# Performance work log

Hardware: AMD Instinct MI355X
Metric: run time of the kernel (lower is better)

The kernel has to match this reference:

```python
import jax, jax.numpy as jnp
import numpy as np

B, S, D = 4, 1024, 1024      # batch, seq_len, hidden_size
I = 4096                     # intermediate_size
E = 8                        # num_experts
K = 2                        # top-k


def setup_inputs() -> dict:
    key = jax.random.key(0)
    ks = jax.random.split(key, 8)
    x = jax.random.normal(ks[0], (B, S, D), dtype=jnp.float32)
    gate_w = jax.random.normal(ks[1], (E, D), dtype=jnp.float32) * 0.02
    gate_b = jnp.zeros((E,), dtype=jnp.float32)
    w1 = jax.random.normal(ks[2], (E, I, D), dtype=jnp.float32) * 0.02
    b1 = jnp.zeros((E, I), dtype=jnp.float32)
    w2 = jax.random.normal(ks[3], (E, D, I), dtype=jnp.float32) * 0.02
    b2 = jnp.zeros((E, D), dtype=jnp.float32)
    return {"x": x, "gate_w": gate_w, "gate_b": gate_b,
            "w1": w1, "b1": b1, "w2": w2, "b2": b2}


def reference(x, gate_w, gate_b, w1, b1, w2, b2):
    b, s, d = x.shape
    xf = x.reshape(-1, d)                                  # [N, D]
    logits = xf @ gate_w.T + gate_b                        # [N, E]
    top_vals, top_idx = jax.lax.top_k(logits, K)           # [N, K]
    top_w = jax.nn.softmax(top_vals, axis=-1)              # softmax over the k selected logits

    # combine[n, e] = routing weight of token n for expert e (0 if not selected)
    n_tok = xf.shape[0]
    combine = jnp.zeros((n_tok, w1.shape[0]), dtype=x.dtype)
    combine = combine.at[jnp.arange(n_tok)[:, None], top_idx].add(top_w)

    out = jnp.zeros_like(xf)
    for e in range(w1.shape[0]):                           # small fixed loop over experts
        h = jax.nn.gelu(xf @ w1[e].T + b1[e], approximate=False)  # exact GELU (torch default)
        out = out + combine[:, e:e + 1] * (h @ w2[e].T + b2[e])
    return out.reshape(b, s, d)
```

## Files before the change

### kernel.cpp

```cpp
#include <hip/hip_runtime.h>
#include <math.h>

#define NTOK 4096
#define DDIM 1024
#define IDIM 4096
#define NEXP 8
#define MAXPAD 9216

typedef _Float16 f16x8 __attribute__((ext_vector_type(8)));
typedef _Float16 f16x4 __attribute__((ext_vector_type(4)));
typedef float    f32x4 __attribute__((ext_vector_type(4)));

__device__ __forceinline__ void glds16(const _Float16* g, _Float16* l) {
    __builtin_amdgcn_global_load_lds(
        (const __attribute__((address_space(1))) _Float16*)g,
        (__attribute__((address_space(3))) _Float16*)l, 16, 0, 0);
}

__device__ __forceinline__ float fast_gelu(float v) {
    float u = v * (0.7978845608f + 0.0356774081f * v * v);
    float ex = __builtin_amdgcn_exp2f(u * 2.8853900817779268f);
    float th = 1.0f - 2.0f * __builtin_amdgcn_rcpf(ex + 1.0f);
    return 0.5f * v * (1.0f + th);
}

__global__ void cvt_kernel(const float* __restrict__ src, _Float16* __restrict__ dst, int n4) {
    int i = blockIdx.x * blockDim.x + threadIdx.x;
    if (i >= n4) return;
    float4 v = ((const float4*)src)[i];
    f16x4 o = { (_Float16)v.x, (_Float16)v.y, (_Float16)v.z, (_Float16)v.w };
    ((f16x4*)dst)[i] = o;
}

__global__ void gate_kernel(const float* __restrict__ x, const float* __restrict__ gw,
                            const float* __restrict__ gb,
                            int* __restrict__ cnt, int* __restrict__ tok,
                            float* __restrict__ wgt) {
    int wave = threadIdx.x >> 6;
    int lane = threadIdx.x & 63;
    int token = blockIdx.x * 4 + wave;
    const float* xr = x + (size_t)token * DDIM;
    float xv[16];
#pragma unroll
    for (int j = 0; j < 16; ++j) xv[j] = xr[lane + 64 * j];
    float lg[NEXP];
#pragma unroll
    for (int e = 0; e < NEXP; ++e) {
        const float* g = gw + e * DDIM;
        float s = 0.f;
#pragma unroll
        for (int j = 0; j < 16; ++j) s += xv[j] * g[lane + 64 * j];
#pragma unroll
        for (int o = 32; o > 0; o >>= 1) s += __shfl_xor(s, o, 64);
        lg[e] = s + gb[e];
    }
    if (lane == 0) {
        int i0 = 0; float v0 = lg[0];
        for (int e = 1; e < NEXP; ++e) if (lg[e] > v0) { v0 = lg[e]; i0 = e; }
        int i1 = -1; float v1 = -3.0e38f;
        for (int e = 0; e < NEXP; ++e) { if (e == i0) continue; if (lg[e] > v1) { v1 = lg[e]; i1 = e; } }
        float e1 = expf(v1 - v0);
        float den = 1.f + e1;
        float w0 = 1.f / den;
        float w1 = e1 / den;
        int p0 = atomicAdd(&cnt[i0], 1);
        tok[i0 * NTOK + p0] = token; wgt[i0 * NTOK + p0] = w0;
        int p1 = atomicAdd(&cnt[i1], 1);
        tok[i1 * NTOK + p1] = token; wgt[i1 * NTOK + p1] = w1;
    }
}

__global__ void scan_kernel(const int* __restrict__ cnt, int* __restrict__ off,
                            int* __restrict__ q1, int* __restrict__ q2) {
    if (threadIdx.x == 0) {
        int acc = 0;
        for (int e = 0; e < NEXP; ++e) { off[e] = acc; acc += ((cnt[e] + 127) >> 7) << 7; }
        off[NEXP] = acc;
        int n1 = 0, n2 = 0;
        for (int e = 0; e < NEXP; ++e) {
            int mtiles = (cnt[e] + 255) >> 8;
            for (int mt = 0; mt < mtiles; ++mt) {
                for (int nt = 0; nt < IDIM / 256; ++nt)
                    q1[n1++] = e | (mt << 4) | (nt << 12);
                for (int kc = 0; kc < 4; ++kc)
                    for (int nt = 0; nt < DDIM / 256; ++nt)
                        q2[n2++] = e | (mt << 4) | (nt << 12) | (kc << 20);
            }
        }
        off[10] = n1; off[11] = n2;
    }
}

__global__ void gather_kernel(const float* __restrict__ x, const int* __restrict__ cnt,
                              const int* __restrict__ off, const int* __restrict__ tok,
                              _Float16* __restrict__ xg) {
    int row = blockIdx.x;
    if (row >= off[NEXP]) return;
    int e = 0;
    while (e < NEXP - 1 && row >= off[e + 1]) ++e;
    int r = row - off[e];
    int t = threadIdx.x;
    _Float16* dst = xg + (size_t)row * DDIM;
    if (r < cnt[e]) {
        int token = tok[e * NTOK + r];
        float4 v = ((const float4*)(x + (size_t)token * DDIM))[t];
        f16x4 o = { (_Float16)v.x, (_Float16)v.y, (_Float16)v.z, (_Float16)v.w };
        ((f16x4*)dst)[t] = o;
    } else {
        f16x4 z = {};
        ((f16x4*)dst)[t] = z;
    }
}

#define SBAR() do { __builtin_amdgcn_s_barrier(); asm volatile("" ::: "memory"); } while (0)
#define STA(b, s, ko) glds16(ap[s] + (ko), &As[b][((s) * 64 + wv * 8) * 64])
#define STB(b, s, ko) glds16(bp[s] + (ko), &Bs[b][((s) * 64 + wv * 8) * 64])
#define ARD(buf, row, kb) (*(const f16x8*)&As[buf][(row) * 64 + ((((kb) + fq) ^ ((row) & 7)) << 3)])
#define BRD(buf, row, kb) (*(const f16x8*)&Bs[buf][(row) * 64 + ((((kb) + fq) ^ ((row) & 7)) << 3)])

template <int KDIM, int NDIM, int EPI, int SPLIT>
__global__ __launch_bounds__(512, 2) void gemm256_kernel(
    const _Float16* __restrict__ A,
    const _Float16* __restrict__ Bw,
    const float* __restrict__ bias,
    const int* __restrict__ cnt, const int* __restrict__ off,
    const int* __restrict__ tok, const float* __restrict__ wgt,
    _Float16* __restrict__ Hout, float* __restrict__ Out,
    const int* __restrict__ qarr, const int* __restrict__ qn) {
    constexpr int KB = KDIM / SPLIT;
    constexpr int NK = KB / 64;

    __shared__ __align__(16) _Float16 As[2][256 * 64];
    __shared__ __align__(16) _Float16 Bs[2][256 * 64];

    const int tid = threadIdx.x;
    const int wv = tid >> 6, lane = tid & 63;
    const int wm = (wv >> 2) * 128;
    const int wn = (wv & 3) * 64;
    const int fr = lane & 15, fq = lane >> 4;
    const int srow = lane >> 3;
    const int scol = ((lane & 7) ^ srow) << 3;
    const int nwork = *qn;

    for (int wi = blockIdx.x; wi < nwork; wi += gridDim.x) {
        __syncthreads();
        const int w = qarr[wi];
        const int e  = w & 15;
        const int mt = (w >> 4) & 63;
        const int nt = (w >> 12) & 63;
        const int kc = (w >> 20) & 7;
        const int ce = cnt[e];
        const int rowbase = off[e] + mt * 256;
        const int colbase = nt * 256;

        const _Float16* ap[4];
        const _Float16* bp[4];
#pragma unroll
        for (int s = 0; s < 4; ++s) {
            int ra = rowbase + s * 64 + wv * 8 + srow;
            if (ra > MAXPAD - 1) ra = MAXPAD - 1;
            ap[s] = A + (size_t)ra * KDIM + kc * KB + scol;
            bp[s] = Bw + ((size_t)e * NDIM + colbase + s * 64 + wv * 8 + srow) * KDIM + kc * KB + scol;
        }

        f32x4 acc[8][4] = {};

        STA(0, 0, 0); STA(0, 1, 0); STA(0, 2, 0); STA(0, 3, 0);
        STB(0, 0, 0); STB(0, 1, 0); STB(0, 2, 0); STB(0, 3, 0);

        for (int kt = 0; kt < NK; ++kt) {
            const int cur = kt & 1, nxt = cur ^ 1;
            const int ko = (kt + 1) * 64;
            f16x8 a[4], b[4];
            if (kt + 1 < NK) {
                STA(nxt, 0, ko); STA(nxt, 1, ko); STA(nxt, 2, ko); STA(nxt, 3, ko);
                STB(nxt, 0, ko); STB(nxt, 1, ko); STB(nxt, 2, ko); STB(nxt, 3, ko);
                asm volatile("s_waitcnt vmcnt(8)" ::: "memory");
            } else {
                asm volatile("s_waitcnt vmcnt(0)" ::: "memory");
            }
            SBAR();
#pragma unroll
            for (int i = 0; i < 4; ++i) a[i] = ARD(cur, wm + i * 16 + fr, 0);
#pragma unroll
            for (int j = 0; j < 4; ++j) b[j] = BRD(cur, wn + j * 16 + fr, 0);
            __builtin_amdgcn_s_setprio(1);
#pragma unroll
            for (int i = 0; i < 4; ++i)
#pragma unroll
                for (int j = 0; j < 4; ++j)
                    acc[i][j] = __builtin_amdgcn_mfma_f32_16x16x32_f16(a[i], b[j], acc[i][j], 0, 0, 0);
            __builtin_amdgcn_s_setprio(0);
#pragma unroll
            for (int i = 0; i < 4; ++i) a[i] = ARD(cur, wm + 64 + i * 16 + fr, 0);
            __builtin_amdgcn_s_setprio(1);
#pragma unroll
            for (int i = 0; i < 4; ++i)
#pragma unroll
                for (int j = 0; j < 4; ++j)
                    acc[i + 4][j] = __builtin_amdgcn_mfma_f32_16x16x32_f16(a[i], b[j], acc[i + 4][j], 0, 0, 0);
            __builtin_amdgcn_s_setprio(0);
#pragma unroll
            for (int i = 0; i < 4; ++i) a[i] = ARD(cur, wm + 64 + i * 16 + fr, 4);
#pragma unroll
            for (int j = 0; j < 4; ++j) b[j] = BRD(cur, wn + j * 16 + fr, 4);
            __builtin_amdgcn_s_setprio(1);
#pragma unroll
            for (int i = 0; i < 4; ++i)
#pragma unroll
                for (int j = 0; j < 4; ++j)
                    acc[i + 4][j] = __builtin_amdgcn_mfma_f32_16x16x32_f16(a[i], b[j], acc[i + 4][j], 0, 0, 0);
            __builtin_amdgcn_s_setprio(0);
#pragma unroll
            for (int i = 0; i < 4; ++i) a[i] = ARD(cur, wm + i * 16 + fr, 4);
            __builtin_amdgcn_s_setprio(1);
#pragma unroll
            for (int i = 0; i < 4; ++i)
#pragma unroll
                for (int j = 0; j < 4; ++j)
                    acc[i][j] = __builtin_amdgcn_mfma_f32_16x16x32_f16(a[i], b[j], acc[i][j], 0, 0, 0);
            __builtin_amdgcn_s_setprio(0);
            asm volatile("s_waitcnt lgkmcnt(0)" ::: "memory");
            SBAR();
        }

        const int rq = fq << 2;
        if constexpr (EPI == 1) {
            const int elim = off[e + 1];
#pragma unroll
            for (int q = 0; q < 8; ++q) {
                const int rbase = wm + ((q >> 2) * 64) + ((q & 3) * 16) + rq;
#pragma unroll
                for (int r = 0; r < 4; ++r) {
                    const int grow = rowbase + rbase + r;
                    if (grow < elim) {
#pragma unroll
                        for (int j = 0; j < 4; ++j) {
                            const int col = colbase + wn + j * 16 + fr;
                            float v = fast_gelu(acc[q][j][r] + bias[e * NDIM + col]);
                            Hout[(size_t)grow * NDIM + col] = (_Float16)v;
                        }
                    }
                }
            }
        } else {
#pragma unroll
            for (int q = 0; q < 8; ++q) {
                const int rbase = wm + ((q >> 2) * 64) + ((q & 3) * 16) + rq;
#pragma unroll
                for (int r = 0; r < 4; ++r) {
                    const int slot = mt * 256 + rbase + r;
                    if (slot < ce) {
                        const int token = tok[e * NTOK + slot];
                        const float ww = wgt[e * NTOK + slot];
#pragma unroll
                        for (int j = 0; j < 4; ++j) {
                            const int col = colbase + wn + j * 16 + fr;
                            float v = acc[q][j][r];
                            if (kc == 0) v += bias[e * NDIM + col];
                            unsafeAtomicAdd(&Out[(size_t)token * NDIM + col], ww * v);
                        }
                    }
                }
            }
        }
    }
}

extern "C" void kernel_launch(void* const* d_in, const int* in_sizes, int n_in,
                              void* d_out, int out_size, void* d_ws, size_t ws_size,
                              hipStream_t stream) {
    const float* x      = (const float*)d_in[0];
    const float* gate_w = (const float*)d_in[1];
    const float* gate_b = (const float*)d_in[2];
    const float* w1     = (const float*)d_in[3];
    const float* b1     = (const float*)d_in[4];
    const float* w2     = (const float*)d_in[5];
    const float* b2     = (const float*)d_in[6];
    float* out = (float*)d_out;

    char* p = (char*)d_ws;
    _Float16* w1h  = (_Float16*)p; p += (size_t)NEXP * IDIM * DDIM * 2;
    _Float16* w2h  = (_Float16*)p; p += (size_t)NEXP * DDIM * IDIM * 2;
    _Float16* xg   = (_Float16*)p; p += (size_t)MAXPAD * DDIM * 2;
    _Float16* hbuf = (_Float16*)p; p += (size_t)MAXPAD * IDIM * 2;
    int*      tok  = (int*)p;      p += (size_t)NEXP * NTOK * 4;
    float*    wgt  = (float*)p;    p += (size_t)NEXP * NTOK * 4;
    int*      cnt  = (int*)p;      p += 128;
    int*      off  = (int*)p;      p += 128;
    int*      q1   = (int*)p;      p += 4096;
    int*      q2   = (int*)p;      p += 4096;

    hipMemsetAsync(cnt, 0, 128, stream);
    hipMemsetAsync(out, 0, (size_t)NTOK * DDIM * 4, stream);

    cvt_kernel<<<32768, 256, 0, stream>>>(w1, w1h, NEXP * IDIM * DDIM / 4);
    cvt_kernel<<<32768, 256, 0, stream>>>(w2, w2h, NEXP * DDIM * IDIM / 4);
    gate_kernel<<<NTOK / 4, 256, 0, stream>>>(x, gate_w, gate_b, cnt, tok, wgt);
    scan_kernel<<<1, 64, 0, stream>>>(cnt, off, q1, q2);
    gather_kernel<<<MAXPAD, 256, 0, stream>>>(x, cnt, off, tok, xg);

    gemm256_kernel<DDIM, IDIM, 1, 1><<<dim3(256), 512, 0, stream>>>(
        xg, w1h, b1, cnt, off, tok, wgt, hbuf, (float*)nullptr, q1, off + 10);
    gemm256_kernel<IDIM, DDIM, 2, 4><<<dim3(256), 512, 0, stream>>>(
        hbuf, w2h, b2, cnt, off, tok, wgt, (_Float16*)nullptr, out, q2, off + 11);
}
```

Measured before the change: 842.2 us.

## Use 16-wave blocks with 4-stage K=32 LDS pipeline in expert GEMMs

Restructures the grouped GEMM to launch 1024 threads (16 waves), each owning a 64x64 sub-tile of the 256x256 block instead of 128x64. It also halves the K slice to 32, with a 4-deep ring of LDS buffers and three stages prefetched, using an adjusted XOR swizzle. The aim is to hide global-load latency with deeper prefetch and to cut per-wave accumulator registers for more latency tolerance. In exchange each wave does less MFMA work per barrier, so barriers per unit of work roughly double. The fixed-count vmcnt waits also depend on each wave issuing exactly two loads per stage.

```diff
diff --git a/kernel.cpp b/kernel.cpp
--- a/kernel.cpp
+++ b/kernel.cpp
@@ -113,13 +113,15 @@
 }
 
 #define SBAR() do { __builtin_amdgcn_s_barrier(); asm volatile("" ::: "memory"); } while (0)
-#define STA(b, s, ko) glds16(ap[s] + (ko), &As[b][((s) * 64 + wv * 8) * 64])
-#define STB(b, s, ko) glds16(bp[s] + (ko), &Bs[b][((s) * 64 + wv * 8) * 64])
-#define ARD(buf, row, kb) (*(const f16x8*)&As[buf][(row) * 64 + ((((kb) + fq) ^ ((row) & 7)) << 3)])
-#define BRD(buf, row, kb) (*(const f16x8*)&Bs[buf][(row) * 64 + ((((kb) + fq) ^ ((row) & 7)) << 3)])
+#define STAGE(b, ko) do { \
+    glds16(ap + (ko), &As[b][wv * 512]); \
+    glds16(bp + (ko), &Bs[b][wv * 512]); \
+} while (0)
+#define ARD(buf, r) (*(const f16x8*)&As[buf][(r) * 32 + ((fq ^ (((r) >> 1) & 3)) << 3)])
+#define BRD(buf, r) (*(const f16x8*)&Bs[buf][(r) * 32 + ((fq ^ (((r) >> 1) & 3)) << 3)])
 
 template <int KDIM, int NDIM, int EPI, int SPLIT>
-__global__ __launch_bounds__(512, 2) void gemm256_kernel(
+__global__ __launch_bounds__(1024, 4) void gemm256_kernel(
     const _Float16* __restrict__ A,
     const _Float16* __restrict__ Bw,
     const float* __restrict__ bias,
@@ -128,91 +130,54 @@
     _Float16* __restrict__ Hout, float* __restrict__ Out,
     const int* __restrict__ qarr, const int* __restrict__ qn) {
     constexpr int KB = KDIM / SPLIT;
-    constexpr int NK = KB / 64;
-
-    __shared__ __align__(16) _Float16 As[2][256 * 64];
-    __shared__ __align__(16) _Float16 Bs[2][256 * 64];
+    constexpr int NK = KB / 32;
+
+    __shared__ __align__(16) _Float16 As[4][256 * 32];
+    __shared__ __align__(16) _Float16 Bs[4][256 * 32];
 
     const int tid = threadIdx.x;
     const int wv = tid >> 6, lane = tid & 63;
-    const int wm = (wv >> 2) * 128;
+    const int wm = (wv >> 2) * 64;
     const int wn = (wv & 3) * 64;
     const int fr = lane & 15, fq = lane >> 4;
-    const int srow = lane >> 3;
-    const int scol = ((lane & 7) ^ srow) << 3;
+    const int srow = lane >> 2;
+    const int scol = ((lane & 3) ^ ((lane >> 3) & 3)) << 3;
     const int nwork = *qn;
 
     for (int wi = blockIdx.x; wi < nwork; wi += gridDim.x) {
         __syncthreads();
         const int w = qarr[wi];
         const int e  = w & 15;
-        const int mt = (w >> 4) & 63;
-        const int nt = (w >> 12) & 63;
+        const int mt = (w >> 4) & 255;
+        const int nt = (w >> 12) & 255;
         const int kc = (w >> 20) & 7;
         const int ce = cnt[e];
         const int rowbase = off[e] + mt * 256;
         const int colbase = nt * 256;
 
-        const _Float16* ap[4];
-        const _Float16* bp[4];
-#pragma unroll
-        for (int s = 0; s < 4; ++s) {
-            int ra = rowbase + s * 64 + wv * 8 + srow;
-            if (ra > MAXPAD - 1) ra = MAXPAD - 1;
-            ap[s] = A + (size_t)ra * KDIM + kc * KB + scol;
-            bp[s] = Bw + ((size_t)e * NDIM + colbase + s * 64 + wv * 8 + srow) * KDIM + kc * KB + scol;
-        }
-
-        f32x4 acc[8][4] = {};
-
-        STA(0, 0, 0); STA(0, 1, 0); STA(0, 2, 0); STA(0, 3, 0);
-        STB(0, 0, 0); STB(0, 1, 0); STB(0, 2, 0); STB(0, 3, 0);
+        int ra = rowbase + wv * 16 + srow;
+        if (ra > MAXPAD - 1) ra = MAXPAD - 1;
+        const _Float16* ap = A + (size_t)ra * KDIM + kc * KB + scol;
+        const _Float16* bp = Bw + ((size_t)e * NDIM + colbase + wv * 16 + srow) * KDIM + kc * KB + scol;
+
+        f32x4 acc[4][4] = {};
+
+        STAGE(0, 0); STAGE(1, 32); STAGE(2, 64);
 
         for (int kt = 0; kt < NK; ++kt) {
-            const int cur = kt & 1, nxt = cur ^ 1;
-            const int ko = (kt + 1) * 64;
+            const int buf = kt & 3;
+            if (kt + 3 < NK) STAGE((kt + 3) & 3, (kt + 3) * 32);
+            const int ahead = (NK - 1 - kt) < 3 ? (NK - 1 - kt) : 3;
+            if (ahead == 3)      asm volatile("s_waitcnt vmcnt(6)" ::: "memory");
+            else if (ahead == 2) asm volatile("s_waitcnt vmcnt(4)" ::: "memory");
+            else if (ahead == 1) asm volatile("s_waitcnt vmcnt(2)" ::: "memory");
+            else                 asm volatile("s_waitcnt vmcnt(0)" ::: "memory");
+            SBAR();
             f16x8 a[4], b[4];
-            if (kt + 1 < NK) {
-                STA(nxt, 0, ko); STA(nxt, 1, ko); STA(nxt, 2, ko); STA(nxt, 3, ko);
-                STB(nxt, 0, ko); STB(nxt, 1, ko); STB(nxt, 2, ko); STB(nxt, 3, ko);
-                asm volatile("s_waitcnt vmcnt(8)" ::: "memory");
-            } else {
-                asm volatile("s_waitcnt vmcnt(0)" ::: "memory");
-            }
-            SBAR();
-#pragma unroll
-            for (int i = 0; i < 4; ++i) a[i] = ARD(cur, wm + i * 16 + fr, 0);
-#pragma unroll
-            for (int j = 0; j < 4; ++j) b[j] = BRD(cur, wn + j * 16 + fr, 0);
-            __builtin_amdgcn_s_setprio(1);
-#pragma unroll
-            for (int i = 0; i < 4; ++i)
-#pragma unroll
-                for (int j = 0; j < 4; ++j)
-                    acc[i][j] = __builtin_amdgcn_mfma_f32_16x16x32_f16(a[i], b[j], acc[i][j], 0, 0, 0);
-            __builtin_amdgcn_s_setprio(0);
-#pragma unroll
-            for (int i = 0; i < 4; ++i) a[i] = ARD(cur, wm + 64 + i * 16 + fr, 0);
-            __builtin_amdgcn_s_setprio(1);
-#pragma unroll
-            for (int i = 0; i < 4; ++i)
-#pragma unroll
-                for (int j = 0; j < 4; ++j)
-                    acc[i + 4][j] = __builtin_amdgcn_mfma_f32_16x16x32_f16(a[i], b[j], acc[i + 4][j], 0, 0, 0);
-            __builtin_amdgcn_s_setprio(0);
-#pragma unroll
-            for (int i = 0; i < 4; ++i) a[i] = ARD(cur, wm + 64 + i * 16 + fr, 4);
-#pragma unroll
-            for (int j = 0; j < 4; ++j) b[j] = BRD(cur, wn + j * 16 + fr, 4);
-            __builtin_amdgcn_s_setprio(1);
-#pragma unroll
-            for (int i = 0; i < 4; ++i)
-#pragma unroll
-                for (int j = 0; j < 4; ++j)
-                    acc[i + 4][j] = __builtin_amdgcn_mfma_f32_16x16x32_f16(a[i], b[j], acc[i + 4][j], 0, 0, 0);
-            __builtin_amdgcn_s_setprio(0);
-#pragma unroll
-            for (int i = 0; i < 4; ++i) a[i] = ARD(cur, wm + i * 16 + fr, 4);
+#pragma unroll
+            for (int i = 0; i < 4; ++i) a[i] = ARD(buf, wm + i * 16 + fr);
+#pragma unroll
+            for (int j = 0; j < 4; ++j) b[j] = BRD(buf, wn + j * 16 + fr);
             __builtin_amdgcn_s_setprio(1);
 #pragma unroll
             for (int i = 0; i < 4; ++i)
@@ -228,16 +193,15 @@
         if constexpr (EPI == 1) {
             const int elim = off[e + 1];
 #pragma unroll
-            for (int q = 0; q < 8; ++q) {
-                const int rbase = wm + ((q >> 2) * 64) + ((q & 3) * 16) + rq;
+            for (int i = 0; i < 4; ++i) {
 #pragma unroll
                 for (int r = 0; r < 4; ++r) {
-                    const int grow = rowbase + rbase + r;
+                    const int grow = rowbase + wm + i * 16 + rq + r;
                     if (grow < elim) {
 #pragma unroll
                         for (int j = 0; j < 4; ++j) {
                             const int col = colbase + wn + j * 16 + fr;
-                            float v = fast_gelu(acc[q][j][r] + bias[e * NDIM + col]);
+                            float v = fast_gelu(acc[i][j][r] + bias[e * NDIM + col]);
                             Hout[(size_t)grow * NDIM + col] = (_Float16)v;
                         }
                     }
@@ -245,18 +209,17 @@
             }
         } else {
 #pragma unroll
-            for (int q = 0; q < 8; ++q) {
-                const int rbase = wm + ((q >> 2) * 64) + ((q & 3) * 16) + rq;
+            for (int i = 0; i < 4; ++i) {
 #pragma unroll
                 for (int r = 0; r < 4; ++r) {
-                    const int slot = mt * 256 + rbase + r;
+                    const int slot = mt * 256 + wm + i * 16 + rq + r;
                     if (slot < ce) {
                         const int token = tok[e * NTOK + slot];
                         const float ww = wgt[e * NTOK + slot];
 #pragma unroll
                         for (int j = 0; j < 4; ++j) {
                             const int col = colbase + wn + j * 16 + fr;
-                            float v = acc[q][j][r];
+                            float v = acc[i][j][r];
                             if (kc == 0) v += bias[e * NDIM + col];
                             unsafeAtomicAdd(&Out[(size_t)token * NDIM + col], ww * v);
                         }
@@ -294,14 +257,14 @@
     hipMemsetAsync(cnt, 0, 128, stream);
     hipMemsetAsync(out, 0, (size_t)NTOK * DDIM * 4, stream);
 
+    cvt_kernel<<<32768, 256, 0, stream>>>(w2, w2h, NEXP * DDIM * IDIM / 4);
     cvt_kernel<<<32768, 256, 0, stream>>>(w1, w1h, NEXP * IDIM * DDIM / 4);
-    cvt_kernel<<<32768, 256, 0, stream>>>(w2, w2h, NEXP * DDIM * IDIM / 4);
     gate_kernel<<<NTOK / 4, 256, 0, stream>>>(x, gate_w, gate_b, cnt, tok, wgt);
     scan_kernel<<<1, 64, 0, stream>>>(cnt, off, q1, q2);
     gather_kernel<<<MAXPAD, 256, 0, stream>>>(x, cnt, off, tok, xg);
 
-    gemm256_kernel<DDIM, IDIM, 1, 1><<<dim3(256), 512, 0, stream>>>(
+    gemm256_kernel<DDIM, IDIM, 1, 1><<<dim3(256), 1024, 0, stream>>>(
         xg, w1h, b1, cnt, off, tok, wgt, hbuf, (float*)nullptr, q1, off + 10);
-    gemm256_kernel<IDIM, DDIM, 2, 4><<<dim3(256), 512, 0, stream>>>(
+    gemm256_kernel<IDIM, DDIM, 2, 4><<<dim3(256), 1024, 0, stream>>>(
         hbuf, w2h, b2, cnt, off, tok, wgt, (_Float16*)nullptr, out, q2, off + 11);
 }
```

New measurement: 781.0 us. -7.3%, faster.
